# Kernel optimization log

Hardware: AMD Instinct MI355X
Metric: run time of the kernel (lower is better)

The kernel has to match this reference:

```python
import jax, jax.numpy as jnp
import numpy as np

N = 25000      # nodes
E = 400000     # edges (before self loops)
G = 64         # graphs in batch
H = 16         # attention heads
ITER = 10      # stacked main GATv2 layers


def setup_inputs():
    key = jax.random.key(0)
    c = [0]
    def nk():
        c[0] += 1
        return jax.random.fold_in(key, c[0])
    def glorot(shape):
        fan = shape[-2] + shape[-1]
        return jax.random.normal(nk(), shape, jnp.float32) * np.float32(np.sqrt(2.0 / fan))
    inp = {
        "x": jax.random.normal(nk(), (N, 2), jnp.float32),
        "edge_attr": jax.random.normal(nk(), (E, 2), jnp.float32),
        "edge_index": jax.random.randint(nk(), (2, E), 0, N, jnp.int32),
        "mask": jax.random.randint(nk(), (N,), 0, 2, jnp.int32),
        "batch": jnp.sort(jax.random.randint(nk(), (N,), 0, G, jnp.int32)),
        # gcn: GATv2Conv(2, 4, heads=16, edge_dim=2), concat -> 64
        "g0_Wl": glorot((2, 64)), "g0_bl": jnp.zeros((64,), jnp.float32),
        "g0_Wr": glorot((2, 64)), "g0_br": jnp.zeros((64,), jnp.float32),
        "g0_We": glorot((2, 64)), "g0_att": glorot((H, 4)),
        "g0_bias": jnp.zeros((64,), jnp.float32),
        "bn_gamma": jnp.ones((64,), jnp.float32),
        "bn_beta": jnp.zeros((64,), jnp.float32),
        "m_Wl": glorot((ITER, 64, 64)), "m_bl": jnp.zeros((ITER, 64), jnp.float32),
        "m_Wr": glorot((ITER, 64, 64)), "m_br": jnp.zeros((ITER, 64), jnp.float32),
        "m_We": glorot((ITER, 2, 64)), "m_att": glorot((ITER, H, 4)),
        "m_bias": jnp.zeros((ITER, 64), jnp.float32),
        # final: GATv2Conv(64, 1, heads=16, concat=False)
        "f_Wl": glorot((64, 16)), "f_bl": jnp.zeros((16,), jnp.float32),
        "f_Wr": glorot((64, 16)), "f_br": jnp.zeros((16,), jnp.float32),
        "f_We": glorot((2, 16)), "f_att": glorot((H, 1)),
        "f_bias": jnp.zeros((1,), jnp.float32),
        # sbs: GATv2Conv(64, 1, heads=16, concat=False)
        "s_Wl": glorot((64, 16)), "s_bl": jnp.zeros((16,), jnp.float32),
        "s_Wr": glorot((64, 16)), "s_br": jnp.zeros((16,), jnp.float32),
        "s_We": glorot((2, 16)), "s_att": glorot((H, 1)),
        "s_bias": jnp.zeros((1,), jnp.float32),
    }
    return inp


def _gatv2(x, src, dst, eattr, Wl, bl, Wr, br, We, att, bias, concat):
    """PyG GATv2Conv: x_l[j]+x_r[i]+e -> LeakyReLU(0.2) -> att dot -> segment softmax over dst."""
    n = x.shape[0]
    h, c = att.shape
    xl = (x @ Wl + bl).reshape(n, h, c)
    xr = (x @ Wr + br).reshape(n, h, c)
    e = (eattr @ We).reshape(-1, h, c)
    m = jax.nn.leaky_relu(xl[src] + xr[dst] + e, 0.2)          # [Etot,H,C]
    logit = jnp.einsum('ehc,hc->eh', m, att)                    # [Etot,H]
    lmax = jax.ops.segment_max(logit, dst, num_segments=n)
    ex = jnp.exp(logit - lmax[dst])
    den = jax.ops.segment_sum(ex, dst, num_segments=n)
    alpha = ex / den[dst]
    out = jax.ops.segment_sum(xl[src] * alpha[..., None], dst, num_segments=n)  # [N,H,C]
    out = out.reshape(n, h * c) if concat else out.mean(axis=1)
    return out + bias


def reference(x, edge_attr, edge_index, mask, batch,
              g0_Wl, g0_bl, g0_Wr, g0_br, g0_We, g0_att, g0_bias,
              bn_gamma, bn_beta,
              m_Wl, m_bl, m_Wr, m_br, m_We, m_att, m_bias,
              f_Wl, f_bl, f_Wr, f_br, f_We, f_att, f_bias,
              s_Wl, s_bl, s_Wr, s_br, s_We, s_att, s_bias):
    n = x.shape[0]
    src, dst = edge_index[0], edge_index[1]
    # add self loops; self-loop edge attr = mean of incoming edge attrs (fill_value='mean')
    ones = jnp.ones((src.shape[0],), jnp.float32)
    cnt = jax.ops.segment_sum(ones, dst, num_segments=n)
    esum = jax.ops.segment_sum(edge_attr, dst, num_segments=n)
    loop_attr = esum / jnp.maximum(cnt, 1.0)[:, None]
    arng = jnp.arange(n, dtype=edge_index.dtype)
    src2 = jnp.concatenate([src, arng])
    dst2 = jnp.concatenate([dst, arng])
    ea2 = jnp.concatenate([edge_attr, loop_attr], axis=0)

    h0 = _gatv2(x, src2, dst2, ea2, g0_Wl, g0_bl, g0_Wr, g0_br, g0_We, g0_att, g0_bias, True)
    mu = h0.mean(axis=0)
    var = h0.var(axis=0)
    h = jax.nn.leaky_relu((h0 - mu) * jax.lax.rsqrt(var + 1e-5) * bn_gamma + bn_beta, 0.01)

    def step(hc, p):
        Wl, bl, Wr, br, We, att, bias = p
        hc = jax.nn.leaky_relu(_gatv2(hc, src2, dst2, ea2, Wl, bl, Wr, br, We, att, bias, True), 0.01)
        return hc, None
    h, _ = jax.lax.scan(step, h, (m_Wl, m_bl, m_Wr, m_br, m_We, m_att, m_bias))

    mus = _gatv2(h, src2, dst2, ea2, s_Wl, s_bl, s_Wr, s_br, s_We, s_att, s_bias, False)[:, 0]  # [N]
    fin = _gatv2(h, src2, dst2, ea2, f_Wl, f_bl, f_Wr, f_br, f_We, f_att, f_bias, False)        # [N,1]
    w = (mask == 0).astype(jnp.float32)
    sums = jax.ops.segment_sum(fin * w[:, None], batch, num_segments=G)
    cnts = jax.ops.segment_sum(w, batch, num_segments=G)
    sat = (sums / jnp.maximum(cnts, 1.0)[:, None])[:, 0]  # [G]
    return mus, sat
```

## Files before the change

### kernel.cpp

```cpp
#include <hip/hip_runtime.h>
#include <hip/hip_fp16.h>


static __device__ __forceinline__ float lrelu(float x, float s) {
    return fmaxf(x, s * x);
}

__global__ void k_build0(const int* __restrict__ dst, int* __restrict__ cnt,
                         int* __restrict__ rank, int E) {
    int idx = blockIdx.x * blockDim.x + threadIdx.x;
    if (idx < E) rank[idx] = atomicAdd(&cnt[dst[idx]], 1);
}

__global__ void k_segoff(const int* __restrict__ cnt, int* __restrict__ row_start,
                         int* __restrict__ cursor, int n) {
    int i = blockIdx.x * blockDim.x + threadIdx.x;
    int lane = threadIdx.x & 63;
    int v = (i < n) ? cnt[i] : 0;
    int s = v;
#pragma unroll
    for (int off = 1; off < 64; off <<= 1) {
        int t = __shfl_up(s, off);
        if (lane >= off) s += t;
    }
    int wavetot = __shfl(s, 63);
    int base = 0;
    if (lane == 63) base = atomicAdd(cursor, wavetot);
    base = __shfl(base, 63);
    if (i < n) row_start[i] = base + s - v;
}

__global__ void k_scatter(const int* __restrict__ src, const int* __restrict__ dst,
                          const float* __restrict__ ea, const int* __restrict__ rank,
                          const int* __restrict__ row_start,
                          int* __restrict__ csr_src, float* __restrict__ csr_ea, int E) {
    int e = blockIdx.x * blockDim.x + threadIdx.x;
    if (e >= E) return;
    int pos = row_start[dst[e]] + rank[e];
    csr_src[pos] = src[e];
    *(float2*)(csr_ea + 2 * (size_t)pos) = *(const float2*)(ea + 2 * (size_t)e);
}

__launch_bounds__(256, 8)
__global__ void k_gat0(const float* __restrict__ x,
                       const int* __restrict__ row_start, const int* __restrict__ cnt,
                       const int* __restrict__ csr_src, const float* __restrict__ csr_ea,
                       const float* __restrict__ Wl, const float* __restrict__ bl,
                       const float* __restrict__ Wr, const float* __restrict__ br,
                       const float* __restrict__ We, const float* __restrict__ att,
                       const float* __restrict__ bias,
                       float* __restrict__ out, int n) {
    int d = (blockIdx.x * blockDim.x + threadIdx.x) >> 6;
    int lane = threadIdx.x & 63;
    if (d >= n) return;
    const int p0 = __builtin_amdgcn_readfirstlane(row_start[d]);
    const int deg = __builtin_amdgcn_readfirstlane(cnt[d]);
    const int p1 = p0 + deg;
    const float wl0 = Wl[lane], wl1 = Wl[64 + lane], blv = bl[lane];
    const float we0 = We[lane], we1 = We[64 + lane];
    const float av = att[lane];
    const float2 xd = *(const float2*)(x + 2 * (size_t)d);
    const float xrv = fmaf(xd.x, Wr[lane], fmaf(xd.y, Wr[64 + lane], br[lane]));

    float den0 = 0.f, acc0 = 0.f;
    float den1 = 0.f, acc1 = 0.f;
    float s0 = 0.f, s1 = 0.f;

    auto step = [&](float xv, float2 ea, bool valid, float& den, float& acc) {
        float vm = valid ? 1.f : 0.f;
        s0 = fmaf(vm, ea.x, s0);
        s1 = fmaf(vm, ea.y, s1);
        float tv = lrelu(xv + xrv + ea.x * we0 + ea.y * we1, 0.2f) * av;
        tv += __shfl_xor(tv, 1);
        tv += __shfl_xor(tv, 2);
        if (!valid) tv = -__builtin_inff();
        float w = __expf(tv);
        den += w;
        acc += w * xv;
    };

    for (int p = p0; p < p1; p += 4) {
        int q1 = min(p + 1, p1 - 1), q2 = min(p + 2, p1 - 1), q3 = min(p + 3, p1 - 1);
        int e0s = csr_src[p], e1s = csr_src[q1], e2s = csr_src[q2], e3s = csr_src[q3];
        float2 ea0 = *(const float2*)(csr_ea + 2 * (size_t)p);
        float2 ea1 = *(const float2*)(csr_ea + 2 * (size_t)q1);
        float2 ea2 = *(const float2*)(csr_ea + 2 * (size_t)q2);
        float2 ea3 = *(const float2*)(csr_ea + 2 * (size_t)q3);
        float2 xs0 = *(const float2*)(x + 2 * (size_t)e0s);
        float2 xs1 = *(const float2*)(x + 2 * (size_t)e1s);
        float2 xs2 = *(const float2*)(x + 2 * (size_t)e2s);
        float2 xs3 = *(const float2*)(x + 2 * (size_t)e3s);
        float xv0 = fmaf(xs0.x, wl0, fmaf(xs0.y, wl1, blv));
        float xv1 = fmaf(xs1.x, wl0, fmaf(xs1.y, wl1, blv));
        float xv2 = fmaf(xs2.x, wl0, fmaf(xs2.y, wl1, blv));
        float xv3 = fmaf(xs3.x, wl0, fmaf(xs3.y, wl1, blv));
        step(xv0, ea0, true, den0, acc0);
        step(xv1, ea1, p + 1 < p1, den1, acc1);
        step(xv2, ea2, p + 2 < p1, den0, acc0);
        step(xv3, ea3, p + 3 < p1, den1, acc1);
    }
    {
        float c = fmaxf((float)deg, 1.f);
        float se0 = s0 / c, se1 = s1 / c;
        float xv = fmaf(xd.x, wl0, fmaf(xd.y, wl1, blv));
        float tv = lrelu(xv + xrv + se0 * we0 + se1 * we1, 0.2f) * av;
        tv += __shfl_xor(tv, 1);
        tv += __shfl_xor(tv, 2);
        float w = __expf(tv);
        den0 += w;
        acc0 += w * xv;
    }
    out[((size_t)d << 6) + lane] = (acc0 + acc1) / (den0 + den1) + bias[lane];
}

__launch_bounds__(256)
__global__ void k_proj64(const float* __restrict__ h,
                         const float* __restrict__ Wl, const float* __restrict__ bl,
                         const float* __restrict__ Wr, const float* __restrict__ br,
                         const double* __restrict__ stats,
                         const float* __restrict__ bng, const float* __restrict__ bnb,
                         __half* __restrict__ xl, float* __restrict__ xr, int n) {
    __shared__ float wsl[4096], wsr[4096], bna[64], bnbb[64];
    int t = threadIdx.x;
    for (int i = t; i < 4096; i += 256) { wsl[i] = Wl[i]; wsr[i] = Wr[i]; }
    if (t < 64) {
        double mu = stats[t] / n;
        double var = stats[64 + t] / n - mu * mu;
        float rs = (float)(1.0 / sqrt(var + 1e-5));
        float a = rs * bng[t];
        bna[t] = a;
        bnbb[t] = bnb[t] - (float)mu * a;
    }
    __syncthreads();
    int rg = t >> 2, cg4 = (t & 3) << 4;
    int r0 = blockIdx.x * 128 + rg * 2;
    float accl[2][16], accr[2][16];
#pragma unroll
    for (int r = 0; r < 2; ++r)
#pragma unroll
        for (int j = 0; j < 16; ++j) { accl[r][j] = 0.f; accr[r][j] = 0.f; }
    for (int k0 = 0; k0 < 64; k0 += 4) {
        float hk[2][4];
#pragma unroll
        for (int r = 0; r < 2; ++r) {
            int gr = r0 + r;
            float4 v = (gr < n) ? *(const float4*)(h + (size_t)gr * 64 + k0)
                                : make_float4(0.f, 0.f, 0.f, 0.f);
            hk[r][0] = v.x; hk[r][1] = v.y; hk[r][2] = v.z; hk[r][3] = v.w;
#pragma unroll
            for (int kk = 0; kk < 4; ++kk)
                hk[r][kk] = lrelu(hk[r][kk] * bna[k0 + kk] + bnbb[k0 + kk], 0.01f);
        }
#pragma unroll
        for (int kk = 0; kk < 4; ++kk) {
            const float* wl = wsl + (k0 + kk) * 64 + cg4;
            const float* wr = wsr + (k0 + kk) * 64 + cg4;
#pragma unroll
            for (int r = 0; r < 2; ++r)
#pragma unroll
                for (int j = 0; j < 16; ++j) {
                    accl[r][j] += hk[r][kk] * wl[j];
                    accr[r][j] += hk[r][kk] * wr[j];
                }
        }
    }
#pragma unroll
    for (int r = 0; r < 2; ++r) {
        int gr = r0 + r;
        if (gr < n) {
            __half* ol = xl + (size_t)gr * 64 + cg4;
            float* orr = xr + (size_t)gr * 64 + cg4;
#pragma unroll
            for (int j = 0; j < 16; ++j) {
                ol[j] = __float2half_rn(accl[r][j] + bl[cg4 + j]);
                orr[j] = accr[r][j] + br[cg4 + j];
            }
        }
    }
}

__device__ __forceinline__ float gat_node(const __half* __restrict__ xl,
                                          const float* __restrict__ xr,
                                          const int* __restrict__ row_start,
                                          const int* __restrict__ cnt,
                                          const int* __restrict__ csr_src,
                                          const float* __restrict__ csr_ea,
                                          const float* __restrict__ We,
                                          const float* __restrict__ att,
                                          const float* __restrict__ bias,
                                          int d, int lane, int relu) {
    const int p0 = __builtin_amdgcn_readfirstlane(row_start[d]);
    const int deg = __builtin_amdgcn_readfirstlane(cnt[d]);
    const int p1 = p0 + deg;
    const float we0 = We[lane], we1 = We[64 + lane];
    const float av = att[lane];
    const float xrv = xr[((size_t)d << 6) + lane];

    float den0 = 0.f, acc0 = 0.f;
    float den1 = 0.f, acc1 = 0.f;
    float s0 = 0.f, s1 = 0.f;

    auto step = [&](float xv, float2 ea, bool valid, float& den, float& acc) {
        float vm = valid ? 1.f : 0.f;
        s0 = fmaf(vm, ea.x, s0);
        s1 = fmaf(vm, ea.y, s1);
        float tv = lrelu(xv + xrv + ea.x * we0 + ea.y * we1, 0.2f) * av;
        tv += __shfl_xor(tv, 1);
        tv += __shfl_xor(tv, 2);
        if (!valid) tv = -__builtin_inff();
        float w = __expf(tv);
        den += w;
        acc += w * xv;
    };

    for (int p = p0; p < p1; p += 4) {
        int q1 = min(p + 1, p1 - 1), q2 = min(p + 2, p1 - 1), q3 = min(p + 3, p1 - 1);
        int e0s = csr_src[p], e1s = csr_src[q1], e2s = csr_src[q2], e3s = csr_src[q3];
        float2 e0 = *(const float2*)(csr_ea + 2 * (size_t)p);
        float2 e1 = *(const float2*)(csr_ea + 2 * (size_t)q1);
        float2 e2 = *(const float2*)(csr_ea + 2 * (size_t)q2);
        float2 e3 = *(const float2*)(csr_ea + 2 * (size_t)q3);
        float x0 = __half2float(xl[((size_t)e0s << 6) + lane]);
        float x1 = __half2float(xl[((size_t)e1s << 6) + lane]);
        float x2 = __half2float(xl[((size_t)e2s << 6) + lane]);
        float x3 = __half2float(xl[((size_t)e3s << 6) + lane]);
        step(x0, e0, true, den0, acc0);
        step(x1, e1, p + 1 < p1, den1, acc1);
        step(x2, e2, p + 2 < p1, den0, acc0);
        step(x3, e3, p + 3 < p1, den1, acc1);
    }
    {
        float c = fmaxf((float)deg, 1.f);
        float se0 = s0 / c, se1 = s1 / c;
        float xv = __half2float(xl[((size_t)d << 6) + lane]);
        float tv = lrelu(xv + xrv + se0 * we0 + se1 * we1, 0.2f) * av;
        tv += __shfl_xor(tv, 1);
        tv += __shfl_xor(tv, 2);
        float w = __expf(tv);
        den0 += w;
        acc0 += w * xv;
    }
    float o = (acc0 + acc1) / (den0 + den1) + bias[lane];
    if (relu) o = lrelu(o, 0.01f);
    return o;
}

__launch_bounds__(64, 8)
__global__ void k_gat_proj2(const __half* __restrict__ xl, const float* __restrict__ xr,
                            const int* __restrict__ row_start, const int* __restrict__ cnt,
                            const int* __restrict__ csr_src, const float* __restrict__ csr_ea,
                            const float* __restrict__ We, const float* __restrict__ att,
                            const float* __restrict__ bias,
                            const float* __restrict__ Wnl, const float* __restrict__ bnl,
                            const float* __restrict__ Wnr, const float* __restrict__ bnr,
                            __half* __restrict__ xl_out, float* __restrict__ xr_out, int n) {
    int wave = blockIdx.x;
    int lane = threadIdx.x & 63;
    int d0 = wave * 2, d1 = d0 + 1;
    if (d0 >= n) return;
    float o0 = gat_node(xl, xr, row_start, cnt, csr_src, csr_ea, We, att, bias, d0, lane, 1);
    float o1 = (d1 < n)
                   ? gat_node(xl, xr, row_start, cnt, csr_src, csr_ea, We, att, bias, d1, lane, 1)
                   : 0.f;
    float al0a = 0.f, al0b = 0.f, ar0a = 0.f, ar0b = 0.f;
    float al1a = 0.f, al1b = 0.f, ar1a = 0.f, ar1b = 0.f;
#pragma unroll 4
    for (int k = 0; k < 64; k += 2) {
        float h0a = __shfl(o0, k), h0b = __shfl(o0, k + 1);
        float h1a = __shfl(o1, k), h1b = __shfl(o1, k + 1);
        float wl0 = Wnl[k * 64 + lane], wl1 = Wnl[(k + 1) * 64 + lane];
        float wr0 = Wnr[k * 64 + lane], wr1 = Wnr[(k + 1) * 64 + lane];
        al0a += h0a * wl0; al0b += h0b * wl1;
        ar0a += h0a * wr0; ar0b += h0b * wr1;
        al1a += h1a * wl0; al1b += h1b * wl1;
        ar1a += h1a * wr0; ar1b += h1b * wr1;
    }
    float bL = bnl[lane], bR = bnr[lane];
    xl_out[((size_t)d0 << 6) + lane] = __float2half_rn(al0a + al0b + bL);
    xr_out[((size_t)d0 << 6) + lane] = ar0a + ar0b + bR;
    if (d1 < n) {
        xl_out[((size_t)d1 << 6) + lane] = __float2half_rn(al1a + al1b + bL);
        xr_out[((size_t)d1 << 6) + lane] = ar1a + ar1b + bR;
    }
}

__launch_bounds__(64, 8)
__global__ void k_gat_projfin2(const __half* __restrict__ xl, const float* __restrict__ xr,
                               const int* __restrict__ row_start, const int* __restrict__ cnt,
                               const int* __restrict__ csr_src, const float* __restrict__ csr_ea,
                               const float* __restrict__ We, const float* __restrict__ att,
                               const float* __restrict__ bias,
                               const float* __restrict__ fWl, const float* __restrict__ fbl,
                               const float* __restrict__ fWr, const float* __restrict__ fbr,
                               const float* __restrict__ sWl, const float* __restrict__ sbl,
                               const float* __restrict__ sWr, const float* __restrict__ sbr,
                               float* __restrict__ packed, int n) {
    int wave = blockIdx.x;
    int lane = threadIdx.x & 63;
    int d0 = wave * 2, d1 = d0 + 1;
    if (d0 >= n) return;
    float o0 = gat_node(xl, xr, row_start, cnt, csr_src, csr_ea, We, att, bias, d0, lane, 1);
    float o1 = (d1 < n)
                   ? gat_node(xl, xr, row_start, cnt, csr_src, csr_ea, We, att, bias, d1, lane, 1)
                   : 0.f;
    int q = lane >> 4, cc = lane & 15;
    const float* W = (q == 0) ? fWl : (q == 1) ? sWl : (q == 2) ? fWr : sWr;
    const float* B = (q == 0) ? fbl : (q == 1) ? sbl : (q == 2) ? fbr : sbr;
    float a0 = 0.f, a1 = 0.f, b0 = 0.f, b1 = 0.f;
#pragma unroll 4
    for (int k = 0; k < 64; k += 2) {
        float w0 = W[k * 16 + cc], w1 = W[(k + 1) * 16 + cc];
        a0 += __shfl(o0, k) * w0;
        a1 += __shfl(o0, k + 1) * w1;
        b0 += __shfl(o1, k) * w0;
        b1 += __shfl(o1, k + 1) * w1;
    }
    float bb = B[cc];
    packed[((size_t)d0 << 6) + lane] = a0 + a1 + bb;
    if (d1 < n) packed[((size_t)d1 << 6) + lane] = b0 + b1 + bb;
}

__launch_bounds__(256)
__global__ void k_gat_final(const float* __restrict__ packed,
                            const int* __restrict__ row_start, const int* __restrict__ cnt,
                            const int* __restrict__ csr_src, const float* __restrict__ csr_ea,
                            const float* __restrict__ fWe, const float* __restrict__ sWe,
                            const float* __restrict__ fatt, const float* __restrict__ satt,
                            const float* __restrict__ fbias, const float* __restrict__ sbias,
                            float* __restrict__ fin, float* __restrict__ mus, int n) {
    int hw = (blockIdx.x * blockDim.x + threadIdx.x) >> 5;
    if (hw >= n) return;
    int l = threadIdx.x & 31;
    int hh = l & 15, sel = l >> 4;
    const int d = hw;
    const int p0 = row_start[d], deg = cnt[d], p1 = p0 + deg;
    const float* We = sel ? sWe : fWe;
    float we0 = We[hh], we1 = We[16 + hh];
    float av = (sel ? satt : fatt)[hh];
    float xrv = packed[(size_t)d * 64 + 32 + sel * 16 + hh];
    int xli = sel * 16 + hh;

    float den0 = 0.f, acc0 = 0.f;
    float den1 = 0.f, acc1 = 0.f;
    float s0 = 0.f, s1 = 0.f;

    auto step = [&](float xv, float2 ea, bool valid, float& den, float& acc) {
        float vm = valid ? 1.f : 0.f;
        s0 = fmaf(vm, ea.x, s0);
        s1 = fmaf(vm, ea.y, s1);
        float t = lrelu(xv + xrv + ea.x * we0 + ea.y * we1, 0.2f) * av;
        if (!valid) t = -__builtin_inff();
        float w = __expf(t);
        den += w;
        acc += w * xv;
    };

    for (int p = p0; p < p1; p += 4) {
        int q1 = min(p + 1, p1 - 1), q2 = min(p + 2, p1 - 1), q3 = min(p + 3, p1 - 1);
        int e0s = csr_src[p], e1s = csr_src[q1], e2s = csr_src[q2], e3s = csr_src[q3];
        float2 e0 = *(const float2*)(csr_ea + 2 * (size_t)p);
        float2 e1 = *(const float2*)(csr_ea + 2 * (size_t)q1);
        float2 e2 = *(const float2*)(csr_ea + 2 * (size_t)q2);
        float2 e3 = *(const float2*)(csr_ea + 2 * (size_t)q3);
        float x0 = packed[(size_t)e0s * 64 + xli];
        float x1 = packed[(size_t)e1s * 64 + xli];
        float x2 = packed[(size_t)e2s * 64 + xli];
        float x3 = packed[(size_t)e3s * 64 + xli];
        step(x0, e0, true, den0, acc0);
        step(x1, e1, p + 1 < p1, den1, acc1);
        step(x2, e2, p + 2 < p1, den0, acc0);
        step(x3, e3, p + 3 < p1, den1, acc1);
    }
    {
        float c = fmaxf((float)deg, 1.f);
        float se0 = s0 / c, se1 = s1 / c;
        float xv = packed[(size_t)d * 64 + xli];
        float t = lrelu(xv + xrv + se0 * we0 + se1 * we1, 0.2f) * av;
        float w = __expf(t);
        den0 += w;
        acc0 += w * xv;
    }
    float val = (acc0 + acc1) / (den0 + den1);
#pragma unroll
    for (int w = 1; w < 16; w <<= 1) val += __shfl_xor(val, w);
    if ((threadIdx.x & 15) == 0) {
        float o = val * (1.f / 16.f) + (sel ? sbias[0] : fbias[0]);
        if (sel) mus[d] = o; else fin[d] = o;
    }
}


__global__ void k_bnstats(const float* __restrict__ h, double* __restrict__ stats, int n) {
    int c = threadIdx.x & 63;
    int s0 = blockIdx.x * (blockDim.x >> 6) + (threadIdx.x >> 6);
    int ns = gridDim.x * (blockDim.x >> 6);
    double s = 0.0, s2 = 0.0;
    for (int i = s0; i < n; i += ns) {
        float v = h[(size_t)i * 64 + c];
        s += v;
        s2 += (double)v * v;
    }
    atomicAdd(&stats[c], s);
    atomicAdd(&stats[64 + c], s2);
}


__global__ void k_sat_acc(const float* __restrict__ fin, const int* __restrict__ mask,
                          const int* __restrict__ batch,
                          float* __restrict__ sums, float* __restrict__ cnts, int n) {
    int i = blockIdx.x * blockDim.x + threadIdx.x;
    int lane = threadIdx.x & 63;
    int g = (i < n) ? batch[i] : -1;
    float c = (i < n && mask[i] == 0) ? 1.f : 0.f;
    float v = (c > 0.f) ? fin[i] : 0.f;
#pragma unroll
    for (int off = 1; off < 64; off <<= 1) {
        float v2 = __shfl_down(v, off);
        float c2 = __shfl_down(c, off);
        int g2 = __shfl_down(g, off);
        if (lane + off < 64 && g2 == g) { v += v2; c += c2; }
    }
    int gprev = __shfl_up(g, 1);
    bool head = (lane == 0) || (gprev != g);
    if (head && g >= 0 && c > 0.f) {
        atomicAdd(&sums[g], v);
        atomicAdd(&cnts[g], c);
    }
}

__global__ void k_sat_fin(const float* __restrict__ sums, const float* __restrict__ cnts,
                          float* __restrict__ out, int g) {
    int i = threadIdx.x;
    if (i < g) out[i] = sums[i] / fmaxf(cnts[i], 1.f);
}


extern "C" void kernel_launch(void* const* d_in, const int* in_sizes, int n_in,
                              void* d_out, int out_size, void* d_ws, size_t ws_size,
                              hipStream_t stream) {
    const float* x = (const float*)d_in[0];
    const float* eat = (const float*)d_in[1];
    const int* ei = (const int*)d_in[2];
    const int* mask = (const int*)d_in[3];
    const int* batch = (const int*)d_in[4];
    const float* g0_Wl = (const float*)d_in[5];
    const float* g0_bl = (const float*)d_in[6];
    const float* g0_Wr = (const float*)d_in[7];
    const float* g0_br = (const float*)d_in[8];
    const float* g0_We = (const float*)d_in[9];
    const float* g0_att = (const float*)d_in[10];
    const float* g0_bias = (const float*)d_in[11];
    const float* bn_g = (const float*)d_in[12];
    const float* bn_b = (const float*)d_in[13];
    const float* m_Wl = (const float*)d_in[14];
    const float* m_bl = (const float*)d_in[15];
    const float* m_Wr = (const float*)d_in[16];
    const float* m_br = (const float*)d_in[17];
    const float* m_We = (const float*)d_in[18];
    const float* m_att = (const float*)d_in[19];
    const float* m_bias = (const float*)d_in[20];
    const float* f_Wl = (const float*)d_in[21];
    const float* f_bl = (const float*)d_in[22];
    const float* f_Wr = (const float*)d_in[23];
    const float* f_br = (const float*)d_in[24];
    const float* f_We = (const float*)d_in[25];
    const float* f_att = (const float*)d_in[26];
    const float* f_bias = (const float*)d_in[27];
    const float* s_Wl = (const float*)d_in[28];
    const float* s_bl = (const float*)d_in[29];
    const float* s_Wr = (const float*)d_in[30];
    const float* s_br = (const float*)d_in[31];
    const float* s_We = (const float*)d_in[32];
    const float* s_att = (const float*)d_in[33];
    const float* s_bias = (const float*)d_in[34];

    const int N = in_sizes[3];
    const int E = in_sizes[1] / 2;
    const int G = out_size - N;
    const int ITER = in_sizes[14] / 4096;
    const int* srcp = ei;
    const int* dstp = ei + E;

    char* wsb = (char*)d_ws;
    size_t off = 0;
    auto alloc = [&](size_t b) { void* p = wsb + off; off = (off + b + 255) & ~(size_t)255; return p; };
    int* cnt = (int*)alloc((size_t)N * 4);
    int* cursor = (int*)alloc(256);
    double* stats = (double*)alloc(128 * 8);
    float* sums = (float*)alloc((size_t)G * 4);
    float* cnts = (float*)alloc((size_t)G * 4);
    size_t zero_bytes = off;
    int* rank = (int*)alloc((size_t)E * 4);
    int* row_start = (int*)alloc((size_t)N * 4);
    int* csr_src = (int*)alloc((size_t)(E + 4) * 4);
    float* csr_ea = (float*)alloc((size_t)(E + 4) * 8);
    __half* xlA = (__half*)alloc((size_t)N * 128);
    float* xrA = (float*)alloc((size_t)N * 256);
    __half* xlB = (__half*)alloc((size_t)N * 128);
    float* xrB = (float*)alloc((size_t)N * 256);
    float* hbuf = (float*)alloc((size_t)N * 256);
    float* packed = (float*)alloc((size_t)N * 256);
    float* fin = (float*)alloc((size_t)N * 4);
    (void)ws_size; (void)n_in;

    float* outv = (float*)d_out;

    hipMemsetAsync(d_ws, 0, zero_bytes, stream);
    const int tb = 256;
    const int ggrid = (N * 64 + 255) / 256;
    const int npair = (N + 1) / 2;
    k_build0<<<(E + tb - 1) / tb, tb, 0, stream>>>(dstp, cnt, rank, E);
    k_segoff<<<(N + tb - 1) / tb, tb, 0, stream>>>(cnt, row_start, cursor, N);
    k_scatter<<<(E + tb - 1) / tb, tb, 0, stream>>>(srcp, dstp, eat, rank, row_start,
                                                    csr_src, csr_ea, E);

    k_gat0<<<ggrid, tb, 0, stream>>>(x, row_start, cnt, csr_src, csr_ea,
                                     g0_Wl, g0_bl, g0_Wr, g0_br,
                                     g0_We, g0_att, g0_bias, hbuf, N);
    k_bnstats<<<128, 256, 0, stream>>>(hbuf, stats, N);
    k_proj64<<<(N + 127) / 128, 256, 0, stream>>>(hbuf, m_Wl, m_bl, m_Wr, m_br,
                                                  stats, bn_g, bn_b, xlA, xrA, N);

    __half* cur_l = xlA; float* cur_r = xrA;
    __half* alt_l = xlB; float* alt_r = xrB;
    for (int l = 0; l < ITER; ++l) {
        if (l < ITER - 1) {
            k_gat_proj2<<<npair, 64, 0, stream>>>(cur_l, cur_r, row_start, cnt, csr_src, csr_ea,
                                                  m_We + l * 128, m_att + l * 64, m_bias + l * 64,
                                                  m_Wl + (size_t)(l + 1) * 4096, m_bl + (l + 1) * 64,
                                                  m_Wr + (size_t)(l + 1) * 4096, m_br + (l + 1) * 64,
                                                  alt_l, alt_r, N);
        } else {
            k_gat_projfin2<<<npair, 64, 0, stream>>>(cur_l, cur_r, row_start, cnt, csr_src, csr_ea,
                                                     m_We + l * 128, m_att + l * 64, m_bias + l * 64,
                                                     f_Wl, f_bl, f_Wr, f_br,
                                                     s_Wl, s_bl, s_Wr, s_br,
                                                     packed, N);
        }
        __half* t = cur_l; cur_l = alt_l; alt_l = t;
        float* u = cur_r; cur_r = alt_r; alt_r = u;
    }
    k_gat_final<<<(N * 32 + tb - 1) / tb, tb, 0, stream>>>(packed, row_start, cnt, csr_src, csr_ea,
                                                           f_We, s_We, f_att, s_att,
                                                           f_bias, s_bias, fin, outv, N);
    k_sat_acc<<<(N + tb - 1) / tb, tb, 0, stream>>>(fin, mask, batch, sums, cnts, N);
    k_sat_fin<<<1, 64, 0, stream>>>(sums, cnts, outv + N, G);
}
```

Before: 614.3 us.

## Software-pipeline edge gathers and map one node per wave in GAT layers

The per-node edge loop now double-buffers its loads: the next group of four edge indices, attributes and fp16 features is issued before the current group is consumed, so gather latency overlaps the softmax math. The main and final layer kernels drop the two-nodes-per-wave pairing in favour of one node per wave with 256-thread blocks. Gather addresses switch to 32-bit unsigned arithmetic. The cost is extra live registers for the prefetch buffers, and the projection weights are no longer shared across two nodes per wave.

Measured after the change: 623.0 us. About the same (+1.4%).

```diff
diff --git a/kernel.cpp b/kernel.cpp
--- a/kernel.cpp
+++ b/kernel.cpp
@@ -179,6 +179,30 @@
     }
 }
 
+#define GAT_ISSUE(P, I0, I1, I2, I3, E0, E1, E2, E3, X0, X1, X2, X3)          \
+    do {                                                                      \
+        int q0 = min((P) + 0, p1 - 1), q1 = min((P) + 1, p1 - 1);             \
+        int q2 = min((P) + 2, p1 - 1), q3 = min((P) + 3, p1 - 1);             \
+        I0 = csr_src[q0]; I1 = csr_src[q1];                                   \
+        I2 = csr_src[q2]; I3 = csr_src[q3];                                   \
+        E0 = *(const float2*)(csr_ea + 2 * (size_t)q0);                       \
+        E1 = *(const float2*)(csr_ea + 2 * (size_t)q1);                       \
+        E2 = *(const float2*)(csr_ea + 2 * (size_t)q2);                       \
+        E3 = *(const float2*)(csr_ea + 2 * (size_t)q3);                       \
+        X0 = xl[(unsigned)((I0 << 6) + lane)];                                \
+        X1 = xl[(unsigned)((I1 << 6) + lane)];                                \
+        X2 = xl[(unsigned)((I2 << 6) + lane)];                                \
+        X3 = xl[(unsigned)((I3 << 6) + lane)];                                \
+    } while (0)
+
+#define GAT_CONSUME(P, E0, E1, E2, E3, X0, X1, X2, X3)                        \
+    do {                                                                      \
+        step(__half2float(X0), E0, (P) + 0 < p1, den0, acc0);                 \
+        step(__half2float(X1), E1, (P) + 1 < p1, den1, acc1);                 \
+        step(__half2float(X2), E2, (P) + 2 < p1, den0, acc0);                 \
+        step(__half2float(X3), E3, (P) + 3 < p1, den1, acc1);                 \
+    } while (0)
+
 __device__ __forceinline__ float gat_node(const __half* __restrict__ xl,
                                           const float* __restrict__ xr,
                                           const int* __restrict__ row_start,
@@ -213,22 +237,29 @@
         acc += w * xv;
     };
 
-    for (int p = p0; p < p1; p += 4) {
-        int q1 = min(p + 1, p1 - 1), q2 = min(p + 2, p1 - 1), q3 = min(p + 3, p1 - 1);
-        int e0s = csr_src[p], e1s = csr_src[q1], e2s = csr_src[q2], e3s = csr_src[q3];
-        float2 e0 = *(const float2*)(csr_ea + 2 * (size_t)p);
-        float2 e1 = *(const float2*)(csr_ea + 2 * (size_t)q1);
-        float2 e2 = *(const float2*)(csr_ea + 2 * (size_t)q2);
-        float2 e3 = *(const float2*)(csr_ea + 2 * (size_t)q3);
-        float x0 = __half2float(xl[((size_t)e0s << 6) + lane]);
-        float x1 = __half2float(xl[((size_t)e1s << 6) + lane]);
-        float x2 = __half2float(xl[((size_t)e2s << 6) + lane]);
-        float x3 = __half2float(xl[((size_t)e3s << 6) + lane]);
-        step(x0, e0, true, den0, acc0);
-        step(x1, e1, p + 1 < p1, den1, acc1);
-        step(x2, e2, p + 2 < p1, den0, acc0);
-        step(x3, e3, p + 3 < p1, den1, acc1);
-    }
+    if (deg > 0) {
+        int ia0, ia1, ia2, ia3, ib0, ib1, ib2, ib3;
+        float2 ea0, ea1, ea2, ea3, eb0, eb1, eb2, eb3;
+        __half xa0, xa1, xa2, xa3, xb0, xb1, xb2, xb3;
+        int p = p0;
+        GAT_ISSUE(p, ia0, ia1, ia2, ia3, ea0, ea1, ea2, ea3, xa0, xa1, xa2, xa3);
+        while (p + 4 < p1) {
+            GAT_ISSUE(p + 4, ib0, ib1, ib2, ib3, eb0, eb1, eb2, eb3, xb0, xb1, xb2, xb3);
+            GAT_CONSUME(p, ea0, ea1, ea2, ea3, xa0, xa1, xa2, xa3);
+            p += 4;
+            if (p + 4 < p1) {
+                GAT_ISSUE(p + 4, ia0, ia1, ia2, ia3, ea0, ea1, ea2, ea3, xa0, xa1, xa2, xa3);
+                GAT_CONSUME(p, eb0, eb1, eb2, eb3, xb0, xb1, xb2, xb3);
+                p += 4;
+            } else {
+                GAT_CONSUME(p, eb0, eb1, eb2, eb3, xb0, xb1, xb2, xb3);
+                goto edges_done;
+            }
+        }
+        GAT_CONSUME(p, ea0, ea1, ea2, ea3, xa0, xa1, xa2, xa3);
+    edges_done:;
+    }
+
     {
         float c = fmaxf((float)deg, 1.f);
         float se0 = s0 / c, se1 = s1 / c;
@@ -245,79 +276,58 @@
     return o;
 }
 
-__launch_bounds__(64, 8)
-__global__ void k_gat_proj2(const __half* __restrict__ xl, const float* __restrict__ xr,
-                            const int* __restrict__ row_start, const int* __restrict__ cnt,
-                            const int* __restrict__ csr_src, const float* __restrict__ csr_ea,
-                            const float* __restrict__ We, const float* __restrict__ att,
-                            const float* __restrict__ bias,
-                            const float* __restrict__ Wnl, const float* __restrict__ bnl,
-                            const float* __restrict__ Wnr, const float* __restrict__ bnr,
-                            __half* __restrict__ xl_out, float* __restrict__ xr_out, int n) {
-    int wave = blockIdx.x;
+__launch_bounds__(256, 8)
+__global__ void k_gat_proj(const __half* __restrict__ xl, const float* __restrict__ xr,
+                           const int* __restrict__ row_start, const int* __restrict__ cnt,
+                           const int* __restrict__ csr_src, const float* __restrict__ csr_ea,
+                           const float* __restrict__ We, const float* __restrict__ att,
+                           const float* __restrict__ bias,
+                           const float* __restrict__ Wnl, const float* __restrict__ bnl,
+                           const float* __restrict__ Wnr, const float* __restrict__ bnr,
+                           __half* __restrict__ xl_out, float* __restrict__ xr_out, int n) {
+    int d = (blockIdx.x * blockDim.x + threadIdx.x) >> 6;
     int lane = threadIdx.x & 63;
-    int d0 = wave * 2, d1 = d0 + 1;
-    if (d0 >= n) return;
-    float o0 = gat_node(xl, xr, row_start, cnt, csr_src, csr_ea, We, att, bias, d0, lane, 1);
-    float o1 = (d1 < n)
-                   ? gat_node(xl, xr, row_start, cnt, csr_src, csr_ea, We, att, bias, d1, lane, 1)
-                   : 0.f;
-    float al0a = 0.f, al0b = 0.f, ar0a = 0.f, ar0b = 0.f;
-    float al1a = 0.f, al1b = 0.f, ar1a = 0.f, ar1b = 0.f;
-#pragma unroll 4
+    if (d >= n) return;
+    float o = gat_node(xl, xr, row_start, cnt, csr_src, csr_ea, We, att, bias, d, lane, 1);
+    float a0 = 0.f, a1 = 0.f, b0 = 0.f, b1 = 0.f;
+#pragma unroll 8
     for (int k = 0; k < 64; k += 2) {
-        float h0a = __shfl(o0, k), h0b = __shfl(o0, k + 1);
-        float h1a = __shfl(o1, k), h1b = __shfl(o1, k + 1);
-        float wl0 = Wnl[k * 64 + lane], wl1 = Wnl[(k + 1) * 64 + lane];
-        float wr0 = Wnr[k * 64 + lane], wr1 = Wnr[(k + 1) * 64 + lane];
-        al0a += h0a * wl0; al0b += h0b * wl1;
-        ar0a += h0a * wr0; ar0b += h0b * wr1;
-        al1a += h1a * wl0; al1b += h1b * wl1;
-        ar1a += h1a * wr0; ar1b += h1b * wr1;
-    }
-    float bL = bnl[lane], bR = bnr[lane];
-    xl_out[((size_t)d0 << 6) + lane] = __float2half_rn(al0a + al0b + bL);
-    xr_out[((size_t)d0 << 6) + lane] = ar0a + ar0b + bR;
-    if (d1 < n) {
-        xl_out[((size_t)d1 << 6) + lane] = __float2half_rn(al1a + al1b + bL);
-        xr_out[((size_t)d1 << 6) + lane] = ar1a + ar1b + bR;
-    }
-}
-
-__launch_bounds__(64, 8)
-__global__ void k_gat_projfin2(const __half* __restrict__ xl, const float* __restrict__ xr,
-                               const int* __restrict__ row_start, const int* __restrict__ cnt,
-                               const int* __restrict__ csr_src, const float* __restrict__ csr_ea,
-                               const float* __restrict__ We, const float* __restrict__ att,
-                               const float* __restrict__ bias,
-                               const float* __restrict__ fWl, const float* __restrict__ fbl,
-                               const float* __restrict__ fWr, const float* __restrict__ fbr,
-                               const float* __restrict__ sWl, const float* __restrict__ sbl,
-                               const float* __restrict__ sWr, const float* __restrict__ sbr,
-                               float* __restrict__ packed, int n) {
-    int wave = blockIdx.x;
+        float h0 = __shfl(o, k);
+        float h1 = __shfl(o, k + 1);
+        a0 += h0 * Wnl[k * 64 + lane];
+        a1 += h1 * Wnl[(k + 1) * 64 + lane];
+        b0 += h0 * Wnr[k * 64 + lane];
+        b1 += h1 * Wnr[(k + 1) * 64 + lane];
+    }
+    xl_out[((size_t)d << 6) + lane] = __float2half_rn(a0 + a1 + bnl[lane]);
+    xr_out[((size_t)d << 6) + lane] = b0 + b1 + bnr[lane];
+}
+
+__launch_bounds__(256, 8)
+__global__ void k_gat_projfin(const __half* __restrict__ xl, const float* __restrict__ xr,
+                              const int* __restrict__ row_start, const int* __restrict__ cnt,
+                              const int* __restrict__ csr_src, const float* __restrict__ csr_ea,
+                              const float* __restrict__ We, const float* __restrict__ att,
+                              const float* __restrict__ bias,
+                              const float* __restrict__ fWl, const float* __restrict__ fbl,
+                              const float* __restrict__ fWr, const float* __restrict__ fbr,
+                              const float* __restrict__ sWl, const float* __restrict__ sbl,
+                              const float* __restrict__ sWr, const float* __restrict__ sbr,
+                              float* __restrict__ packed, int n) {
+    int d = (blockIdx.x * blockDim.x + threadIdx.x) >> 6;
     int lane = threadIdx.x & 63;
-    int d0 = wave * 2, d1 = d0 + 1;
-    if (d0 >= n) return;
-    float o0 = gat_node(xl, xr, row_start, cnt, csr_src, csr_ea, We, att, bias, d0, lane, 1);
-    float o1 = (d1 < n)
-                   ? gat_node(xl, xr, row_start, cnt, csr_src, csr_ea, We, att, bias, d1, lane, 1)
-                   : 0.f;
+    if (d >= n) return;
+    float o = gat_node(xl, xr, row_start, cnt, csr_src, csr_ea, We, att, bias, d, lane, 1);
     int q = lane >> 4, cc = lane & 15;
     const float* W = (q == 0) ? fWl : (q == 1) ? sWl : (q == 2) ? fWr : sWr;
     const float* B = (q == 0) ? fbl : (q == 1) ? sbl : (q == 2) ? fbr : sbr;
-    float a0 = 0.f, a1 = 0.f, b0 = 0.f, b1 = 0.f;
-#pragma unroll 4
+    float a0 = 0.f, a1 = 0.f;
+#pragma unroll 8
     for (int k = 0; k < 64; k += 2) {
-        float w0 = W[k * 16 + cc], w1 = W[(k + 1) * 16 + cc];
-        a0 += __shfl(o0, k) * w0;
-        a1 += __shfl(o0, k + 1) * w1;
-        b0 += __shfl(o1, k) * w0;
-        b1 += __shfl(o1, k + 1) * w1;
-    }
-    float bb = B[cc];
-    packed[((size_t)d0 << 6) + lane] = a0 + a1 + bb;
-    if (d1 < n) packed[((size_t)d1 << 6) + lane] = b0 + b1 + bb;
+        a0 += __shfl(o, k) * W[k * 16 + cc];
+        a1 += __shfl(o, k + 1) * W[(k + 1) * 16 + cc];
+    }
+    packed[((size_t)d << 6) + lane] = a0 + a1 + B[cc];
 }
 
 __launch_bounds__(256)
@@ -508,7 +518,6 @@
     hipMemsetAsync(d_ws, 0, zero_bytes, stream);
     const int tb = 256;
     const int ggrid = (N * 64 + 255) / 256;
-    const int npair = (N + 1) / 2;
     k_build0<<<(E + tb - 1) / tb, tb, 0, stream>>>(dstp, cnt, rank, E);
     k_segoff<<<(N + tb - 1) / tb, tb, 0, stream>>>(cnt, row_start, cursor, N);
     k_scatter<<<(E + tb - 1) / tb, tb, 0, stream>>>(srcp, dstp, eat, rank, row_start,
@@ -525,17 +534,17 @@
     __half* alt_l = xlB; float* alt_r = xrB;
     for (int l = 0; l < ITER; ++l) {
         if (l < ITER - 1) {
-            k_gat_proj2<<<npair, 64, 0, stream>>>(cur_l, cur_r, row_start, cnt, csr_src, csr_ea,
-                                                  m_We + l * 128, m_att + l * 64, m_bias + l * 64,
-                                                  m_Wl + (size_t)(l + 1) * 4096, m_bl + (l + 1) * 64,
-                                                  m_Wr + (size_t)(l + 1) * 4096, m_br + (l + 1) * 64,
-                                                  alt_l, alt_r, N);
+            k_gat_proj<<<ggrid, tb, 0, stream>>>(cur_l, cur_r, row_start, cnt, csr_src, csr_ea,
+                                                 m_We + l * 128, m_att + l * 64, m_bias + l * 64,
+                                                 m_Wl + (size_t)(l + 1) * 4096, m_bl + (l + 1) * 64,
+                                                 m_Wr + (size_t)(l + 1) * 4096, m_br + (l + 1) * 64,
+                                                 alt_l, alt_r, N);
         } else {
-            k_gat_projfin2<<<npair, 64, 0, stream>>>(cur_l, cur_r, row_start, cnt, csr_src, csr_ea,
-                                                     m_We + l * 128, m_att + l * 64, m_bias + l * 64,
-                                                     f_Wl, f_bl, f_Wr, f_br,
-                                                     s_Wl, s_bl, s_Wr, s_br,
-                                                     packed, N);
+            k_gat_projfin<<<ggrid, tb, 0, stream>>>(cur_l, cur_r, row_start, cnt, csr_src, csr_ea,
+                                                    m_We + l * 128, m_att + l * 64, m_bias + l * 64,
+                                                    f_Wl, f_bl, f_Wr, f_br,
+                                                    s_Wl, s_bl, s_Wr, s_br,
+                                                    packed, N);
         }
         __half* t = cur_l; cur_l = alt_l; alt_l = t;
         float* u = cur_r; cur_r = alt_r; alt_r = u;
```
